# Kernel tuning notes

Hardware: AMD Instinct MI355X
Metric: run time of the kernel (lower is better)

## Reference

```python
import jax, jax.numpy as jnp
import numpy as np
import math

PAD, DIL, K = 4, 2, 3  # causal dilated conv: pad = dilation*(kernel-1)


def _conv1d_causal(x, w, b):
    # x: [B, C, L], w: [O, I, K]
    y = jax.lax.conv_general_dilated(
        x, w, window_strides=(1,), padding=[(PAD, PAD)], rhs_dilation=(DIL,),
        dimension_numbers=('NCH', 'OIH', 'NCH'))
    return (y + b[None, :, None])[:, :, :-PAD]  # trim trailing pad -> length L


def _attn_weights(x, wq, wk):
    # einsum('jj,ijk->ijk', W, X) == diag(W)[None,:,None] * X
    q = jnp.diagonal(wq)[None, :, None] * x
    k = jnp.diagonal(wk)[None, :, None] * x
    scores = jnp.einsum('bnd,bmd->bnm', q, k) / math.sqrt(x.shape[-1])
    return jax.nn.softmax(scores, axis=-1)  # [B, N, N]


def _gcn(x, A, W, b):
    # GCNConv with dense fully-connected edge weights A[r,c] (src r -> dst c):
    # deg[c] = sum_r A[r,c]; out[c] = sum_r A[r,c]/sqrt(deg[r]deg[c]) * (xW)[r] + b
    deg = A.sum(axis=0)
    safe = jnp.where(deg > 0, deg, 1.0)
    dis = jnp.where(deg > 0, 1.0 / jnp.sqrt(safe), 0.0)
    M = dis[:, None] * A * dis[None, :]  # [N, N]
    return jnp.einsum('rc,brh->bch', M, x @ W) + b


def _forward(X_time, conv_w, conv_b, wq_feat, wk_feat, wq_time, wk_time,
             gf1_w, gf1_b, gf2_w, gf2_b, gf3_w, gf3_b,
             gt1_w, gt1_b, gt2_w, gt2_b, gt3_w, gt3_b, proj_w, proj_b):
    B, Wd, F = X_time.shape
    # NOTE: original uses torch.reshape (not transpose) -- replicate exactly.
    X_feat = X_time.reshape(B, F, Wd)
    X_feat = _conv1d_causal(X_feat, conv_w, conv_b)  # [B, F, Wd]

    A_feat = _attn_weights(X_feat, wq_feat, wk_feat).mean(axis=0)  # [F, F]
    h = _gcn(X_feat, A_feat, gf1_w, gf1_b)
    h = _gcn(h, A_feat, gf2_w, gf2_b)
    h = _gcn(h, A_feat, gf3_w, gf3_b)
    out_feat = h.mean(axis=1)  # [B, H]

    A_time = _attn_weights(X_time, wq_time, wk_time).mean(axis=0)  # [Wd, Wd]
    h = _gcn(X_time, A_time, gt1_w, gt1_b)
    h = _gcn(h, A_time, gt2_w, gt2_b)
    h = _gcn(h, A_time, gt3_w, gt3_b)
    out_time = h.mean(axis=1)  # [B, H]

    out = jnp.concatenate([out_feat, out_time], axis=-1) @ proj_w + proj_b
    return out, A_feat.ravel(), A_time.ravel()


def setup_inputs() -> dict:
    B, Wd, F, H, O = 512, 256, 128, 128, 64
    ks = jax.random.split(jax.random.key(0), 20)
    n = lambda k, s, sc=1.0: (jax.random.normal(k, s, dtype=jnp.float32) * sc)
    return {
        'X_time': n(ks[0], (B, Wd, F)),
        'conv_w': n(ks[1], (F, F, K), 0.05), 'conv_b': jnp.zeros((F,), jnp.float32),
        'wq_feat': n(ks[2], (F, F)), 'wk_feat': n(ks[3], (F, F)),
        'wq_time': n(ks[4], (Wd, Wd)), 'wk_time': n(ks[5], (Wd, Wd)),
        'gf1_w': n(ks[6], (Wd, H), 0.05), 'gf1_b': jnp.zeros((H,), jnp.float32),
        'gf2_w': n(ks[7], (H, H), 0.05), 'gf2_b': jnp.zeros((H,), jnp.float32),
        'gf3_w': n(ks[8], (H, H), 0.05), 'gf3_b': jnp.zeros((H,), jnp.float32),
        'gt1_w': n(ks[9], (F, H), 0.05), 'gt1_b': jnp.zeros((H,), jnp.float32),
        'gt2_w': n(ks[10], (H, H), 0.05), 'gt2_b': jnp.zeros((H,), jnp.float32),
        'gt3_w': n(ks[11], (H, H), 0.05), 'gt3_b': jnp.zeros((H,), jnp.float32),
        'proj_w': n(ks[12], (2 * H, O), 0.05), 'proj_b': jnp.zeros((O,), jnp.float32),
    }


def reference(X_time, conv_w, conv_b, wq_feat, wk_feat, wq_time, wk_time,
              gf1_w, gf1_b, gf2_w, gf2_b, gf3_w, gf3_b,
              gt1_w, gt1_b, gt2_w, gt2_b, gt3_w, gt3_b, proj_w, proj_b):
    return _forward(X_time, conv_w, conv_b, wq_feat, wk_feat, wq_time, wk_time,
                    gf1_w, gf1_b, gf2_w, gf2_b, gf3_w, gf3_b,
                    gt1_w, gt1_b, gt2_w, gt2_b, gt3_w, gt3_b, proj_w, proj_b)
```

## Files before the change

### kernel.cpp

```cpp
#include <hip/hip_runtime.h>
#include <hip/hip_bf16.h>

#define NB 512
#define WD 256
#define NF 128

typedef __attribute__((ext_vector_type(8))) short short8v;
typedef __attribute__((ext_vector_type(4))) float f32x4;

__device__ inline unsigned pk2bf(float a, float b) {
  __hip_bfloat162 h;
  h.x = __float2bfloat16(a);
  h.y = __float2bfloat16(b);
  unsigned r;
  __builtin_memcpy(&r, &h, 4);
  return r;
}

__device__ inline float bf2f(unsigned short u) {
  unsigned v = (unsigned)u << 16;
  float f;
  __builtin_memcpy(&f, &v, 4);
  return f;
}

__global__ __launch_bounds__(256) void prep_x(
    const float* __restrict__ X, __hip_bfloat16* __restrict__ Xflat,
    __hip_bfloat16* __restrict__ Xt)
{
  __shared__ float tile[32][33];
  int b = blockIdx.y, tt = blockIdx.x;
  int i0 = (tt >> 3) * 32, l0 = (tt & 7) * 32;
  const float* Xb = X + (size_t)b * 32768;
  __hip_bfloat16* Fb = Xflat + (size_t)b * 32768;
  __hip_bfloat16* Tb = Xt + (size_t)b * 32768;
  int t = threadIdx.x;
  {
    int r = t >> 3, c4 = t & 7;
    float4 v = *(const float4*)(Xb + (size_t)(i0 + r) * 256 + l0 + c4 * 4);
    uint2 p;
    p.x = pk2bf(v.x, v.y);
    p.y = pk2bf(v.z, v.w);
    *(uint2*)(Fb + (size_t)(i0 + r) * 256 + l0 + c4 * 4) = p;
    tile[r][c4 * 4 + 0] = v.x;
    tile[r][c4 * 4 + 1] = v.y;
    tile[r][c4 * 4 + 2] = v.z;
    tile[r][c4 * 4 + 3] = v.w;
  }
  __syncthreads();
  {
    int cr = t >> 3, ch = t & 7;
    float a0 = tile[ch * 4 + 0][cr];
    float a1 = tile[ch * 4 + 1][cr];
    float a2 = tile[ch * 4 + 2][cr];
    float a3 = tile[ch * 4 + 3][cr];
    uint2 q;
    q.x = pk2bf(a0, a1);
    q.y = pk2bf(a2, a3);
    *(uint2*)(Tb + (size_t)(l0 + cr) * 128 + i0 + ch * 4) = q;
  }
}

__global__ void wc_cast(const float* __restrict__ W, __hip_bfloat16* __restrict__ Wc)
{
  int idx = blockIdx.x * 256 + threadIdx.x;
  int o = idx / 384, rem = idx - o * 384;
  int k = rem >> 7, i = rem & 127;
  Wc[idx] = __float2bfloat16(W[(size_t)o * 384 + i * 3 + k]);
}

__global__ __launch_bounds__(256) void conv_gemm(
    const __hip_bfloat16* __restrict__ Xt, const __hip_bfloat16* __restrict__ Wc,
    const float* __restrict__ bias, __hip_bfloat16* __restrict__ Out)
{
  __shared__ unsigned short ldsA[2][4096];
  __shared__ unsigned short ldsB[2][4096];
  int b = blockIdx.y;
  int trt = blockIdx.x;
  int t = threadIdx.x, l = t & 63, w = t >> 6;
  int wr = (w >> 1) * 64, wcc = (w & 1) * 64;
  int lr = l & 15, lg = l >> 4;
  const __hip_bfloat16* Ab = Xt + (size_t)b * 32768;
  f32x4 acc[4][4] = {};

#define CSTAGE(buf, ks)                                                               \
  {                                                                                   \
    int kgrp = (ks) >> 2;                                                             \
    int kk = ((ks) & 3) * 32 + lg * 8;                                                \
    _Pragma("unroll") for (int ff = 0; ff < 2; ++ff) {                                \
      int f = 2 * w + ff;                                                             \
      int lrow = trt * 128 + f * 16 + lr + 2 * kgrp - 4;                              \
      uint4 ga = make_uint4(0, 0, 0, 0);                                              \
      if (lrow >= 0) ga = *(const uint4*)(Ab + (size_t)lrow * 128 + kk);              \
      *(uint4*)&ldsA[buf][f * 512 + l * 8] = ga;                                      \
      *(uint4*)&ldsB[buf][f * 512 + l * 8] =                                          \
          *(const uint4*)(Wc + (size_t)(f * 16 + lr) * 384 + (ks) * 32 + lg * 8);     \
    }                                                                                 \
  }

  CSTAGE(0, 0)
  __syncthreads();
  for (int ks = 0; ks < 12; ++ks) {
    int buf = ks & 1;
    if (ks + 1 < 12) CSTAGE((ks + 1) & 1, ks + 1)
    short8v a[4], bq[4];
#pragma unroll
    for (int i = 0; i < 4; ++i)
      a[i] = *(const short8v*)&ldsA[buf][((wr >> 4) + i) * 512 + l * 8];
#pragma unroll
    for (int j = 0; j < 4; ++j)
      bq[j] = *(const short8v*)&ldsB[buf][((wcc >> 4) + j) * 512 + l * 8];
#pragma unroll
    for (int i = 0; i < 4; ++i)
#pragma unroll
      for (int j = 0; j < 4; ++j)
        acc[i][j] = __builtin_amdgcn_mfma_f32_16x16x32_bf16(a[i], bq[j], acc[i][j], 0, 0, 0);
    __syncthreads();
  }

  __hip_bfloat16* Ob = Out + (size_t)b * 32768;
#pragma unroll
  for (int i = 0; i < 4; ++i) {
#pragma unroll
    for (int j = 0; j < 4; ++j) {
      int r = trt * 128 + wr + i * 16 + lg * 4;
      int c = wcc + j * 16 + lr;
      f32x4 v = acc[i][j];
      float bv = bias[c];
      uint2 p;
      p.x = pk2bf(v[0] + bv, v[1] + bv);
      p.y = pk2bf(v[2] + bv, v[3] + bv);
      *(uint2*)(Ob + (size_t)c * 256 + r) = p;
    }
  }
}

template <int N, int D, int BPG>
__global__ __launch_bounds__(512) void gram_acc(
    const __hip_bfloat16* __restrict__ X, const float* __restrict__ Wq,
    const float* __restrict__ Wk, __hip_bfloat16* __restrict__ partial, float scale)
{
  constexpr int NT = N / 16;
  constexpr int KS = D / 32;
  constexpr int C8 = D / 8;
  __shared__ char lds[N * D * 2];
  int t = threadIdx.x, l = t & 63, w = t >> 6;
  int lr = l & 15, lg = l >> 4;
  int rowbase = blockIdx.x * 128 + w * 16;
  int swz = (lr & 7) << 4;

  float dkr[NT];
#pragma unroll
  for (int m = 0; m < NT; ++m) dkr[m] = Wk[(size_t)(m * 16 + lr) * (N + 1)] * scale;
  float dqr[4];
#pragma unroll
  for (int i = 0; i < 4; ++i) dqr[i] = Wq[(size_t)(rowbase + lg * 4 + i) * (N + 1)];

  float sumA[4][NT] = {};

#pragma unroll 1
  for (int g = 0; g < BPG; ++g) {
    const __hip_bfloat16* Xb = X + (size_t)(blockIdx.y * BPG + g) * N * D;
    __syncthreads();
    for (int chunk = t; chunk < N * C8; chunk += 512) {
      int row = chunk / C8, c8 = chunk - row * C8;
      int off = row * (2 * D) + ((c8 * 16) ^ ((row & 7) << 4));
      *(uint4*)(lds + off) = *(const uint4*)(Xb + (size_t)row * D + c8 * 8);
    }
    __syncthreads();

    f32x4 acc[NT] = {};
#pragma unroll
    for (int ks = 0; ks < KS; ++ks) {
      int coff = (ks * 64 + lg * 16) ^ swz;
      short8v a = *(const short8v*)(lds + (rowbase + lr) * (2 * D) + coff);
#pragma unroll
      for (int m = 0; m < NT; ++m) {
        short8v bb = *(const short8v*)(lds + (m * 16 + lr) * (2 * D) + coff);
        acc[m] = __builtin_amdgcn_mfma_f32_16x16x32_bf16(a, bb, acc[m], 0, 0, 0);
      }
    }

#pragma unroll
    for (int i = 0; i < 4; ++i) {
      float v[NT];
      float mx = -3.0e38f;
#pragma unroll
      for (int m = 0; m < NT; ++m) {
        v[m] = acc[m][i] * dqr[i] * dkr[m];
        mx = fmaxf(mx, v[m]);
      }
#pragma unroll
      for (int off = 1; off < 16; off <<= 1) mx = fmaxf(mx, __shfl_xor(mx, off));
      float sum = 0.f;
#pragma unroll
      for (int m = 0; m < NT; ++m) { v[m] = __expf(v[m] - mx); sum += v[m]; }
#pragma unroll
      for (int off = 1; off < 16; off <<= 1) sum += __shfl_xor(sum, off);
      float inv = 1.0f / sum;
#pragma unroll
      for (int m = 0; m < NT; ++m) sumA[i][m] += v[m] * inv;
    }
  }

  __hip_bfloat16* Pp = partial + (size_t)blockIdx.y * N * N;
#pragma unroll
  for (int i = 0; i < 4; ++i) {
    int row = rowbase + lg * 4 + i;
#pragma unroll
    for (int m = 0; m < NT; ++m)
      Pp[(size_t)row * N + m * 16 + lr] = __float2bfloat16(sumA[i][m]);
  }
}

__global__ __launch_bounds__(256) void reduce_g(
    const __hip_bfloat16* __restrict__ partial, float* __restrict__ l2, int NN, int GS)
{
  int idx = (blockIdx.x * 256 + threadIdx.x) * 8;
  const __hip_bfloat16* p = partial + (size_t)blockIdx.y * GS * NN + idx;
  float a[8] = {};
#pragma unroll 4
  for (int g = 0; g < GS; ++g) {
    uint4 u = *(const uint4*)(p + (size_t)g * NN);
    unsigned arr[4] = {u.x, u.y, u.z, u.w};
#pragma unroll
    for (int q = 0; q < 4; ++q) {
      a[2 * q] += bf2f((unsigned short)(arr[q] & 0xffff));
      a[2 * q + 1] += bf2f((unsigned short)(arr[q] >> 16));
    }
  }
  float* dst = l2 + (size_t)blockIdx.y * NN + idx;
  *(float4*)dst = make_float4(a[0], a[1], a[2], a[3]);
  *(float4*)(dst + 4) = make_float4(a[4], a[5], a[6], a[7]);
}

__global__ void A_fin(const float* __restrict__ partial, float* __restrict__ A1,
                      float* __restrict__ A2, int NN, int G)
{
  int idx = (blockIdx.x * 256 + threadIdx.x) * 4;
  float4 a = make_float4(0.f, 0.f, 0.f, 0.f);
  for (int g = 0; g < G; ++g) {
    float4 v = *(const float4*)(partial + (size_t)g * NN + idx);
    a.x += v.x; a.y += v.y; a.z += v.z; a.w += v.w;
  }
  a.x *= (1.0f / NB); a.y *= (1.0f / NB); a.z *= (1.0f / NB); a.w *= (1.0f / NB);
  *(float4*)(A1 + idx) = a;
  *(float4*)(A2 + idx) = a;
}

__global__ __launch_bounds__(256) void deg_both(
    const float* __restrict__ Af, const float* __restrict__ At,
    float* __restrict__ disf, float* __restrict__ dist)
{
  __shared__ float red[4][64];
  int bid = blockIdx.x;
  int branch = bid >= 2;
  int N = branch ? 256 : 128;
  const float* A = branch ? At : Af;
  float* dis = branch ? dist : disf;
  int cb = (branch ? (bid - 2) : bid) * 64;
  int t = threadIdx.x, lane = t & 63, rg = t >> 6;
  float s = 0.f;
  for (int r = rg; r < N; r += 4) s += A[(size_t)r * N + cb + lane];
  red[rg][lane] = s;
  __syncthreads();
  if (t < 64) {
    float d = red[0][t] + red[1][t] + red[2][t] + red[3][t];
    dis[cb + t] = (d > 0.f) ? (1.0f / sqrtf(d)) : 0.0f;
  }
}

__global__ __launch_bounds__(256) void mv_both(
    const float* __restrict__ Af, const float* __restrict__ At,
    const float* __restrict__ vf, const float* __restrict__ vt,
    const float* __restrict__ disf, const float* __restrict__ dist,
    float* __restrict__ aof, float* __restrict__ aot,
    float* __restrict__ wof, float* __restrict__ wot, int doScale)
{
  int bid = blockIdx.x;
  int branch = bid >= 32;
  int N = branch ? 256 : 128;
  const float* A = branch ? At : Af;
  const float* v = branch ? vt : vf;
  const float* dis = branch ? dist : disf;
  float* ao = branch ? aot : aof;
  float* wo = branch ? wot : wof;
  int r = (branch ? (bid - 32) : bid) * 4 + (threadIdx.x >> 6);
  int lane = threadIdx.x & 63;
  const float* Ar = A + (size_t)r * N;
  float s = 0.f;
  for (int c = lane * 4; c < N; c += 256) {
    float4 av = *(const float4*)(Ar + c);
    s += av.x * v[c] + av.y * v[c + 1] + av.z * v[c + 2] + av.w * v[c + 3];
  }
#pragma unroll
  for (int off = 32; off > 0; off >>= 1) s += __shfl_xor(s, off);
  if (lane == 0) {
    float a = dis[r] * s;
    float scale = doScale ? (branch ? (1.0f / 256.0f) : (1.0f / 128.0f)) : 1.0f;
    ao[r] = a * scale;
    wo[r] = dis[r] * a;
  }
}

__global__ __launch_bounds__(256) void sum_both(
    const float* __restrict__ af, const float* __restrict__ at,
    float* __restrict__ sv, int idx)
{
  __shared__ float part[4];
  int branch = blockIdx.x;
  int N = branch ? 256 : 128;
  const float* a = branch ? at : af;
  int t = threadIdx.x, lane = t & 63, w = t >> 6;
  float x = (t < N) ? a[t] : 0.f;
#pragma unroll
  for (int off = 32; off > 0; off >>= 1) x += __shfl_xor(x, off);
  if (lane == 0) part[w] = x;
  __syncthreads();
  if (t == 0) sv[branch * 2 + idx] = part[0] + part[1] + part[2] + part[3];
}

__global__ __launch_bounds__(256) void qchain(
    const float* __restrict__ Af, const float* __restrict__ At,
    const float* __restrict__ Bf, const float* __restrict__ Bt,
    float* __restrict__ Cf, float* __restrict__ Ct, int Mf, int Mt)
{
  int branch = blockIdx.y;
  const float* A = branch ? At : Af;
  const float* B = branch ? Bt : Bf;
  float* C = branch ? Ct : Cf;
  int M = branch ? Mt : Mf;
  int r = blockIdx.x * 4 + (threadIdx.x >> 6);
  int o = threadIdx.x & 63;
  if (r >= M) return;
  const float* Ar = A + (size_t)r * 128;
  float s = 0.f;
#pragma unroll 8
  for (int k = 0; k < 128; k += 4) {
    float4 wv = *(const float4*)(Ar + k);
    s += wv.x * B[k * 64 + o] + wv.y * B[(k + 1) * 64 + o] +
         wv.z * B[(k + 2) * 64 + o] + wv.w * B[(k + 3) * 64 + o];
  }
  C[(size_t)r * 64 + o] = s;
}

__global__ __launch_bounds__(128) void bias_fold(
    const float* __restrict__ gf1b, const float* __restrict__ gf2w, const float* __restrict__ gf2b,
    const float* __restrict__ gf3w, const float* __restrict__ gf3b,
    const float* __restrict__ gt1b, const float* __restrict__ gt2w, const float* __restrict__ gt2b,
    const float* __restrict__ gt3w, const float* __restrict__ gt3b,
    const float* __restrict__ projw, const float* __restrict__ sv,
    float* __restrict__ cb)
{
  int branch = blockIdx.x;
  int N = branch ? 256 : 128;
  const float* W2 = branch ? gt2w : gf2w;
  const float* W3 = branch ? gt3w : gf3w;
  const float* b1 = branch ? gt1b : gf1b;
  const float* b2 = branch ? gt2b : gf2b;
  const float* b3 = branch ? gt3b : gf3b;
  const float* P = projw + (size_t)branch * 128 * 64;
  float s1 = sv[branch * 2 + 0], s2 = sv[branch * 2 + 1];
  __shared__ float r1[128], cf[128];
  int t = threadIdx.x;

  {
    float s = 0.f;
#pragma unroll 4
    for (int h = 0; h < 128; ++h) s += b1[h] * W2[(size_t)h * 128 + t];
    r1[t] = s;
  }
  __syncthreads();
  {
    float sa = 0.f, sb = 0.f;
#pragma unroll 4
    for (int h = 0; h < 128; ++h) {
      float w3v = W3[(size_t)h * 128 + t];
      sa += r1[h] * w3v;
      sb += b2[h] * w3v;
    }
    cf[t] = (s2 * sa + s1 * sb) * (1.0f / N) + b3[t];
  }
  __syncthreads();
  if (t < 64) {
    float s = 0.f;
#pragma unroll 4
    for (int h = 0; h < 128; ++h) s += cf[h] * P[(size_t)h * 64 + t];
    cb[branch * 64 + t] = s;
  }
}

__global__ __launch_bounds__(256) void gcn_out(
    const __hip_bfloat16* __restrict__ XF, const __hip_bfloat16* __restrict__ Xt,
    const float* __restrict__ uf, const float* __restrict__ ut,
    const float* __restrict__ Qf, const float* __restrict__ Qt,
    const float* __restrict__ cb, const float* __restrict__ pb,
    float* __restrict__ out)
{
  __shared__ float red[2048];
  __shared__ float yfL[256], ytL[128], red3[4][64];
  int b = blockIdx.x, t = threadIdx.x;

  {
    int rr = t >> 5, cc = t & 31;
    const __hip_bfloat16* base = XF + (size_t)b * 32768;
    float acc[8] = {};
    for (int it = 0; it < 16; ++it) {
      int row = it * 8 + rr;
      float uw = uf[row];
      uint4 v = *(const uint4*)(base + (size_t)row * 256 + cc * 8);
      unsigned arr[4] = {v.x, v.y, v.z, v.w};
#pragma unroll
      for (int q = 0; q < 4; ++q) {
        acc[2 * q] += uw * bf2f((unsigned short)(arr[q] & 0xffff));
        acc[2 * q + 1] += uw * bf2f((unsigned short)(arr[q] >> 16));
      }
    }
#pragma unroll
    for (int j = 0; j < 8; ++j) red[rr * 256 + cc * 8 + j] = acc[j];
  }
  __syncthreads();
  {
    float s = 0.f;
#pragma unroll
    for (int g = 0; g < 8; ++g) s += red[g * 256 + t];
    yfL[t] = s;
  }
  __syncthreads();
  {
    int rr = t >> 4, cc = t & 15;
    const __hip_bfloat16* base = Xt + (size_t)b * 32768;
    float acc[8] = {};
    for (int it = 0; it < 16; ++it) {
      int row = it * 16 + rr;
      float uw = ut[row];
      uint4 v = *(const uint4*)(base + (size_t)row * 128 + cc * 8);
      unsigned arr[4] = {v.x, v.y, v.z, v.w};
#pragma unroll
      for (int q = 0; q < 4; ++q) {
        acc[2 * q] += uw * bf2f((unsigned short)(arr[q] & 0xffff));
        acc[2 * q + 1] += uw * bf2f((unsigned short)(arr[q] >> 16));
      }
    }
#pragma unroll
    for (int j = 0; j < 8; ++j) red[rr * 128 + cc * 8 + j] = acc[j];
  }
  __syncthreads();
  if (t < 128) {
    float s = 0.f;
#pragma unroll
    for (int g = 0; g < 16; ++g) s += red[g * 128 + t];
    ytL[t] = s;
  }
  __syncthreads();
  {
    int grp = t >> 6, o = t & 63;
    float s = 0.f;
    for (int jj = 0; jj < 64; ++jj) {
      int j = grp * 64 + jj;
      s += yfL[j] * Qf[(size_t)j * 64 + o];
    }
    for (int jj = 0; jj < 32; ++jj) {
      int j = grp * 32 + jj;
      s += ytL[j] * Qt[(size_t)j * 64 + o];
    }
    red3[grp][o] = s;
  }
  __syncthreads();
  if (t < 64) {
    out[(size_t)b * 64 + t] = red3[0][t] + red3[1][t] + red3[2][t] + red3[3][t] +
                              pb[t] + cb[t] + cb[64 + t];
  }
}

extern "C" void kernel_launch(void* const* d_in, const int* in_sizes, int n_in,
                              void* d_out, int out_size, void* d_ws, size_t ws_size,
                              hipStream_t stream)
{
  const float* X_time = (const float*)d_in[0];
  const float* conv_w = (const float*)d_in[1];
  const float* conv_b = (const float*)d_in[2];
  const float* wq_feat = (const float*)d_in[3];
  const float* wk_feat = (const float*)d_in[4];
  const float* wq_time = (const float*)d_in[5];
  const float* wk_time = (const float*)d_in[6];
  const float* gf1_w = (const float*)d_in[7];
  const float* gf1_b = (const float*)d_in[8];
  const float* gf2_w = (const float*)d_in[9];
  const float* gf2_b = (const float*)d_in[10];
  const float* gf3_w = (const float*)d_in[11];
  const float* gf3_b = (const float*)d_in[12];
  const float* gt1_w = (const float*)d_in[13];
  const float* gt1_b = (const float*)d_in[14];
  const float* gt2_w = (const float*)d_in[15];
  const float* gt2_b = (const float*)d_in[16];
  const float* gt3_w = (const float*)d_in[17];
  const float* gt3_b = (const float*)d_in[18];
  const float* proj_w = (const float*)d_in[19];
  const float* proj_b = (const float*)d_in[20];

  typedef __hip_bfloat16 bf16;
  char* ws = (char*)d_ws;
  const size_t MiB = 1ull << 20;
  bf16* XFb = (bf16*)ws;
  bf16* Xtb = (bf16*)(ws + 34 * MiB);
  bf16* partial_f = (bf16*)(ws + 68 * MiB);
  bf16* partial_t = (bf16*)(ws + 100 * MiB);
  bf16* Xt = (bf16*)(ws + 100 * MiB);
  float* l2f = (float*)(ws + 164 * MiB);
  float* l2t = (float*)(ws + 166 * MiB);
  char* SM = ws + 171 * MiB;
  float* A_feat = (float*)SM;
  float* A_time = (float*)(SM + 65536);
  float* uf = (float*)(SM + 327680);
  float* ut = (float*)(SM + 328704);
  float* sv = (float*)(SM + 329728);
  float* Qf = (float*)(SM + 331776);
  float* Qt = (float*)(SM + 397312);
  float* cb = (float*)(SM + 430080);
  bf16* Wcv = (bf16*)(SM + 432128);
  float* S3f = (float*)(SM + 530432);
  float* S3t = (float*)(SM + 563200);
  float* S2f = (float*)(SM + 595968);
  float* S2t = (float*)(SM + 628736);
  float* dis_f = (float*)(SM + 661504);
  float* dis_t = (float*)(SM + 662528);
  float* a1f = (float*)(SM + 663552);
  float* a1t = (float*)(SM + 664576);
  float* a2f = (float*)(SM + 665600);
  float* a2t = (float*)(SM + 666624);
  float* w1f = (float*)(SM + 667648);
  float* w1t = (float*)(SM + 668672);
  float* w2f = (float*)(SM + 669696);
  float* w2t = (float*)(SM + 670720);
  float* wdf = (float*)(SM + 671744);
  float* wdt = (float*)(SM + 672768);

  float* out = (float*)d_out;
  float* outA_f = out + 32768;
  float* outA_t = out + 49152;

  prep_x<<<dim3(32, NB), 256, 0, stream>>>(X_time, Xtb, Xt);
  wc_cast<<<192, 256, 0, stream>>>(conv_w, Wcv);
  conv_gemm<<<dim3(2, NB), 256, 0, stream>>>(Xt, Wcv, conv_b, XFb);
  gram_acc<128, 256, 1><<<dim3(1, 512), 512, 0, stream>>>(XFb, wq_feat, wk_feat,
                                                          partial_f, 0.0625f);
  gram_acc<256, 128, 2><<<dim3(2, 256), 512, 0, stream>>>(Xtb, wq_time, wk_time,
                                                          partial_t, 0.08838834764831845f);
  reduce_g<<<dim3(8, 16), 256, 0, stream>>>(partial_f, l2f, 16384, 32);
  reduce_g<<<dim3(32, 16), 256, 0, stream>>>(partial_t, l2t, 65536, 16);
  A_fin<<<16, 256, 0, stream>>>(l2f, A_feat, outA_f, 16384, 16);
  A_fin<<<64, 256, 0, stream>>>(l2t, A_time, outA_t, 65536, 16);
  deg_both<<<6, 256, 0, stream>>>(A_feat, A_time, dis_f, dis_t);
  mv_both<<<96, 256, 0, stream>>>(A_feat, A_time, dis_f, dis_t, dis_f, dis_t,
                                  a1f, a1t, w1f, w1t, 0);
  sum_both<<<2, 256, 0, stream>>>(a1f, a1t, sv, 0);
  mv_both<<<96, 256, 0, stream>>>(A_feat, A_time, w1f, w1t, dis_f, dis_t,
                                  a2f, a2t, w2f, w2t, 0);
  sum_both<<<2, 256, 0, stream>>>(a2f, a2t, sv, 1);
  mv_both<<<96, 256, 0, stream>>>(A_feat, A_time, w2f, w2t, dis_f, dis_t,
                                  uf, ut, wdf, wdt, 1);
  qchain<<<dim3(32, 2), 256, 0, stream>>>(gf3_w, gt3_w, proj_w, proj_w + 8192,
                                          S3f, S3t, 128, 128);
  qchain<<<dim3(32, 2), 256, 0, stream>>>(gf2_w, gt2_w, S3f, S3t, S2f, S2t, 128, 128);
  qchain<<<dim3(64, 2), 256, 0, stream>>>(gf1_w, gt1_w, S2f, S2t, Qf, Qt, 256, 128);
  bias_fold<<<2, 128, 0, stream>>>(gf1_b, gf2_w, gf2_b, gf3_w, gf3_b,
                                   gt1_b, gt2_w, gt2_b, gt3_w, gt3_b,
                                   proj_w, sv, cb);
  gcn_out<<<NB, 256, 0, stream>>>(XFb, Xtb, uf, ut, Qf, Qt, cb, proj_b, out);
}
```

Baseline: 213.7 us.

## Double-buffer LDS in gram_acc with register prefetch and more batches per block

gram_acc now keeps two LDS buffers. It loads the next batch's tile into registers while running MFMA and softmax on the current tile, then stores it to the other buffer, so global loads overlap compute and one sync per batch is dropped. Each block now handles twice as many batches, which halves the grid and the number of bf16 partial matrices; the reduce_g and A_fin group counts are adjusted to match. The LDS footprint doubles to 128KB for both instantiations, which limits residency to one block per CU. It also leaves fewer blocks per launch.

```diff
diff --git a/kernel.cpp b/kernel.cpp
--- a/kernel.cpp
+++ b/kernel.cpp
@@ -143,12 +143,21 @@
   constexpr int NT = N / 16;
   constexpr int KS = D / 32;
   constexpr int C8 = D / 8;
-  __shared__ char lds[N * D * 2];
+  __shared__ char lds[2][N * D * 2];
   int t = threadIdx.x, l = t & 63, w = t >> 6;
   int lr = l & 15, lg = l >> 4;
   int rowbase = blockIdx.x * 128 + w * 16;
   int swz = (lr & 7) << 4;
 
+  int srow[8], soff[8];
+#pragma unroll
+  for (int c = 0; c < 8; ++c) {
+    int chunk = c * 512 + t;
+    int row = chunk / C8, c8 = chunk - row * C8;
+    srow[c] = row * D + c8 * 8;
+    soff[c] = row * (2 * D) + ((c8 * 16) ^ ((row & 7) << 4));
+  }
+
   float dkr[NT];
 #pragma unroll
   for (int m = 0; m < NT; ++m) dkr[m] = Wk[(size_t)(m * 16 + lr) * (N + 1)] * scale;
@@ -158,25 +167,34 @@
 
   float sumA[4][NT] = {};
 
+  {
+    const __hip_bfloat16* Xb = X + (size_t)(blockIdx.y * BPG) * N * D;
+    uint4 r[8];
+#pragma unroll
+    for (int c = 0; c < 8; ++c) r[c] = *(const uint4*)(Xb + srow[c]);
+#pragma unroll
+    for (int c = 0; c < 8; ++c) *(uint4*)(lds[0] + soff[c]) = r[c];
+  }
+  __syncthreads();
+
 #pragma unroll 1
   for (int g = 0; g < BPG; ++g) {
-    const __hip_bfloat16* Xb = X + (size_t)(blockIdx.y * BPG + g) * N * D;
-    __syncthreads();
-    for (int chunk = t; chunk < N * C8; chunk += 512) {
-      int row = chunk / C8, c8 = chunk - row * C8;
-      int off = row * (2 * D) + ((c8 * 16) ^ ((row & 7) << 4));
-      *(uint4*)(lds + off) = *(const uint4*)(Xb + (size_t)row * D + c8 * 8);
-    }
-    __syncthreads();
+    char* cur = lds[g & 1];
+    uint4 rn[8];
+    if (g + 1 < BPG) {
+      const __hip_bfloat16* Xb = X + (size_t)(blockIdx.y * BPG + g + 1) * N * D;
+#pragma unroll
+      for (int c = 0; c < 8; ++c) rn[c] = *(const uint4*)(Xb + srow[c]);
+    }
 
     f32x4 acc[NT] = {};
 #pragma unroll
     for (int ks = 0; ks < KS; ++ks) {
       int coff = (ks * 64 + lg * 16) ^ swz;
-      short8v a = *(const short8v*)(lds + (rowbase + lr) * (2 * D) + coff);
+      short8v a = *(const short8v*)(cur + (rowbase + lr) * (2 * D) + coff);
 #pragma unroll
       for (int m = 0; m < NT; ++m) {
-        short8v bb = *(const short8v*)(lds + (m * 16 + lr) * (2 * D) + coff);
+        short8v bb = *(const short8v*)(cur + (m * 16 + lr) * (2 * D) + coff);
         acc[m] = __builtin_amdgcn_mfma_f32_16x16x32_bf16(a, bb, acc[m], 0, 0, 0);
       }
     }
@@ -200,6 +218,13 @@
       float inv = 1.0f / sum;
 #pragma unroll
       for (int m = 0; m < NT; ++m) sumA[i][m] += v[m] * inv;
+    }
+
+    if (g + 1 < BPG) {
+      char* nxt = lds[(g + 1) & 1];
+#pragma unroll
+      for (int c = 0; c < 8; ++c) *(uint4*)(nxt + soff[c]) = rn[c];
+      __syncthreads();
     }
   }
 
@@ -543,14 +568,14 @@
   prep_x<<<dim3(32, NB), 256, 0, stream>>>(X_time, Xtb, Xt);
   wc_cast<<<192, 256, 0, stream>>>(conv_w, Wcv);
   conv_gemm<<<dim3(2, NB), 256, 0, stream>>>(Xt, Wcv, conv_b, XFb);
-  gram_acc<128, 256, 1><<<dim3(1, 512), 512, 0, stream>>>(XFb, wq_feat, wk_feat,
+  gram_acc<128, 256, 2><<<dim3(1, 256), 512, 0, stream>>>(XFb, wq_feat, wk_feat,
                                                           partial_f, 0.0625f);
-  gram_acc<256, 128, 2><<<dim3(2, 256), 512, 0, stream>>>(Xtb, wq_time, wk_time,
+  gram_acc<256, 128, 4><<<dim3(2, 128), 512, 0, stream>>>(Xtb, wq_time, wk_time,
                                                           partial_t, 0.08838834764831845f);
-  reduce_g<<<dim3(8, 16), 256, 0, stream>>>(partial_f, l2f, 16384, 32);
-  reduce_g<<<dim3(32, 16), 256, 0, stream>>>(partial_t, l2t, 65536, 16);
+  reduce_g<<<dim3(8, 16), 256, 0, stream>>>(partial_f, l2f, 16384, 16);
+  reduce_g<<<dim3(32, 8), 256, 0, stream>>>(partial_t, l2t, 65536, 16);
   A_fin<<<16, 256, 0, stream>>>(l2f, A_feat, outA_f, 16384, 16);
-  A_fin<<<64, 256, 0, stream>>>(l2t, A_time, outA_t, 65536, 16);
+  A_fin<<<64, 256, 0, stream>>>(l2t, A_time, outA_t, 65536, 8);
   deg_both<<<6, 256, 0, stream>>>(A_feat, A_time, dis_f, dis_t);
   mv_both<<<96, 256, 0, stream>>>(A_feat, A_time, dis_f, dis_t, dis_f, dis_t,
                                   a1f, a1t, w1f, w1t, 0);
```

New measurement: 208.1 us. -2.6%, faster.

## Double-buffer gram tiles via async global_load_lds and merge reduction launches

Applied to the files above, without the earlier changes.

The gram kernel now stages each batch tile straight into LDS with global_load_lds into a double buffer, prefetching the next batch while MFMA and softmax run on the current one. Each block handles twice as many batches, which halves the partial buffers, and the diagonal scale vector moves from registers into LDS. The separate feat/time reduce and finalize launches are merged into one launch each. The cost is doubled LDS use per block (occupancy of 1), fewer blocks in flight, and an extra LDS read in the softmax loop.

```diff
diff --git a/kernel.cpp b/kernel.cpp
--- a/kernel.cpp
+++ b/kernel.cpp
@@ -136,47 +136,57 @@
 }
 
 template <int N, int D, int BPG>
-__global__ __launch_bounds__(512) void gram_acc(
+__global__ __launch_bounds__(512, 1) void gram_acc(
     const __hip_bfloat16* __restrict__ X, const float* __restrict__ Wq,
     const float* __restrict__ Wk, __hip_bfloat16* __restrict__ partial, float scale)
 {
   constexpr int NT = N / 16;
   constexpr int KS = D / 32;
   constexpr int C8 = D / 8;
-  __shared__ char lds[N * D * 2];
+  __shared__ char lds[2][N * D * 2];
+  __shared__ float ldsD[N];
   int t = threadIdx.x, l = t & 63, w = t >> 6;
   int lr = l & 15, lg = l >> 4;
   int rowbase = blockIdx.x * 128 + w * 16;
   int swz = (lr & 7) << 4;
 
-  float dkr[NT];
-#pragma unroll
-  for (int m = 0; m < NT; ++m) dkr[m] = Wk[(size_t)(m * 16 + lr) * (N + 1)] * scale;
+  if (t < N) ldsD[t] = Wk[(size_t)t * (N + 1)] * scale;
   float dqr[4];
 #pragma unroll
   for (int i = 0; i < 4; ++i) dqr[i] = Wq[(size_t)(rowbase + lg * 4 + i) * (N + 1)];
 
   float sumA[4][NT] = {};
+
+#define GSTAGE(buf, gb)                                                             \
+  {                                                                                 \
+    const __hip_bfloat16* Xb_ = (gb);                                               \
+    _Pragma("unroll") for (int c = 0; c < 8; ++c) {                                 \
+      int chunk = c * 512 + t;                                                      \
+      int row_ = chunk / C8, j_ = chunk % C8;                                       \
+      int gsrc = row_ * D + ((j_ ^ (row_ & 7)) << 3);                               \
+      __builtin_amdgcn_global_load_lds(                                             \
+          (const __attribute__((address_space(1))) unsigned int*)(const void*)(Xb_ + gsrc), \
+          (__attribute__((address_space(3))) unsigned int*)(void*)(&lds[buf][chunk * 16]),  \
+          16, 0, 0);                                                                \
+    }                                                                               \
+  }
+
+  GSTAGE(0, X + (size_t)(blockIdx.y * BPG) * N * D)
+  __syncthreads();
 
 #pragma unroll 1
   for (int g = 0; g < BPG; ++g) {
-    const __hip_bfloat16* Xb = X + (size_t)(blockIdx.y * BPG + g) * N * D;
-    __syncthreads();
-    for (int chunk = t; chunk < N * C8; chunk += 512) {
-      int row = chunk / C8, c8 = chunk - row * C8;
-      int off = row * (2 * D) + ((c8 * 16) ^ ((row & 7) << 4));
-      *(uint4*)(lds + off) = *(const uint4*)(Xb + (size_t)row * D + c8 * 8);
-    }
-    __syncthreads();
+    if (g + 1 < BPG) GSTAGE((g + 1) & 1, X + (size_t)(blockIdx.y * BPG + g + 1) * N * D)
+    const char* cur = lds[g & 1];
 
     f32x4 acc[NT] = {};
 #pragma unroll
     for (int ks = 0; ks < KS; ++ks) {
       int coff = (ks * 64 + lg * 16) ^ swz;
-      short8v a = *(const short8v*)(lds + (rowbase + lr) * (2 * D) + coff);
+      short8v a = *(const short8v*)(cur + (rowbase + lr) * (2 * D) + coff);
 #pragma unroll
       for (int m = 0; m < NT; ++m) {
-        short8v bb = *(const short8v*)(lds + (m * 16 + lr) * (2 * D) + coff);
+        short8v bb = *(const short8v*)(cur + (m * 16 + lr) * (2 * D) + coff);
         acc[m] = __builtin_amdgcn_mfma_f32_16x16x32_bf16(a, bb, acc[m], 0, 0, 0);
       }
     }
@@ -187,7 +197,7 @@
       float mx = -3.0e38f;
 #pragma unroll
       for (int m = 0; m < NT; ++m) {
-        v[m] = acc[m][i] * dqr[i] * dkr[m];
+        v[m] = acc[m][i] * dqr[i] * ldsD[m * 16 + lr];
         mx = fmaxf(mx, v[m]);
       }
 #pragma unroll
@@ -201,6 +211,8 @@
 #pragma unroll
       for (int m = 0; m < NT; ++m) sumA[i][m] += v[m] * inv;
     }
+
+    if (g + 1 < BPG) __syncthreads();
   }
 
   __hip_bfloat16* Pp = partial + (size_t)blockIdx.y * N * N;
@@ -213,14 +225,21 @@
   }
 }
 
-__global__ __launch_bounds__(256) void reduce_g(
-    const __hip_bfloat16* __restrict__ partial, float* __restrict__ l2, int NN, int GS)
-{
-  int idx = (blockIdx.x * 256 + threadIdx.x) * 8;
-  const __hip_bfloat16* p = partial + (size_t)blockIdx.y * GS * NN + idx;
+__global__ __launch_bounds__(256) void reduce_g2(
+    const __hip_bfloat16* __restrict__ pf, const __hip_bfloat16* __restrict__ pt,
+    float* __restrict__ l2f, float* __restrict__ l2t)
+{
+  int bid = blockIdx.x;
+  const __hip_bfloat16* partial;
+  float* l2;
+  int NN, bx, gy;
+  if (bid < 128) { partial = pf; l2 = l2f; NN = 16384; bx = bid & 7; gy = bid >> 3; }
+  else { int r2 = bid - 128; partial = pt; l2 = l2t; NN = 65536; bx = r2 & 31; gy = r2 >> 5; }
+  int idx = (bx * 256 + threadIdx.x) * 8;
+  const __hip_bfloat16* p = partial + (size_t)gy * 16 * NN + idx;
   float a[8] = {};
 #pragma unroll 4
-  for (int g = 0; g < GS; ++g) {
+  for (int g = 0; g < 16; ++g) {
     uint4 u = *(const uint4*)(p + (size_t)g * NN);
     unsigned arr[4] = {u.x, u.y, u.z, u.w};
 #pragma unroll
@@ -229,18 +248,26 @@
       a[2 * q + 1] += bf2f((unsigned short)(arr[q] >> 16));
     }
   }
-  float* dst = l2 + (size_t)blockIdx.y * NN + idx;
+  float* dst = l2 + (size_t)gy * NN + idx;
   *(float4*)dst = make_float4(a[0], a[1], a[2], a[3]);
   *(float4*)(dst + 4) = make_float4(a[4], a[5], a[6], a[7]);
 }
 
-__global__ void A_fin(const float* __restrict__ partial, float* __restrict__ A1,
-                      float* __restrict__ A2, int NN, int G)
-{
-  int idx = (blockIdx.x * 256 + threadIdx.x) * 4;
+__global__ __launch_bounds__(256) void A_fin2(
+    const float* __restrict__ l2f, const float* __restrict__ l2t,
+    float* __restrict__ A1f, float* __restrict__ A1t,
+    float* __restrict__ A2f, float* __restrict__ A2t)
+{
+  int bid = blockIdx.x;
+  const float* src;
+  float *A1, *A2;
+  int NN, G, ib;
+  if (bid < 16) { src = l2f; A1 = A1f; A2 = A2f; NN = 16384; G = 16; ib = bid; }
+  else { src = l2t; A1 = A1t; A2 = A2t; NN = 65536; G = 8; ib = bid - 16; }
+  int idx = (ib * 256 + threadIdx.x) * 4;
   float4 a = make_float4(0.f, 0.f, 0.f, 0.f);
   for (int g = 0; g < G; ++g) {
-    float4 v = *(const float4*)(partial + (size_t)g * NN + idx);
+    float4 v = *(const float4*)(src + (size_t)g * NN + idx);
     a.x += v.x; a.y += v.y; a.z += v.z; a.w += v.w;
   }
   a.x *= (1.0f / NB); a.y *= (1.0f / NB); a.z *= (1.0f / NB); a.w *= (1.0f / NB);
@@ -543,14 +570,12 @@
   prep_x<<<dim3(32, NB), 256, 0, stream>>>(X_time, Xtb, Xt);
   wc_cast<<<192, 256, 0, stream>>>(conv_w, Wcv);
   conv_gemm<<<dim3(2, NB), 256, 0, stream>>>(Xt, Wcv, conv_b, XFb);
-  gram_acc<128, 256, 1><<<dim3(1, 512), 512, 0, stream>>>(XFb, wq_feat, wk_feat,
+  gram_acc<128, 256, 2><<<dim3(1, 256), 512, 0, stream>>>(XFb, wq_feat, wk_feat,
                                                           partial_f, 0.0625f);
-  gram_acc<256, 128, 2><<<dim3(2, 256), 512, 0, stream>>>(Xtb, wq_time, wk_time,
+  gram_acc<256, 128, 4><<<dim3(2, 128), 512, 0, stream>>>(Xtb, wq_time, wk_time,
                                                           partial_t, 0.08838834764831845f);
-  reduce_g<<<dim3(8, 16), 256, 0, stream>>>(partial_f, l2f, 16384, 32);
-  reduce_g<<<dim3(32, 16), 256, 0, stream>>>(partial_t, l2t, 65536, 16);
-  A_fin<<<16, 256, 0, stream>>>(l2f, A_feat, outA_f, 16384, 16);
-  A_fin<<<64, 256, 0, stream>>>(l2t, A_time, outA_t, 65536, 16);
+  reduce_g2<<<384, 256, 0, stream>>>(partial_f, partial_t, l2f, l2t);
+  A_fin2<<<80, 256, 0, stream>>>(l2f, l2t, A_feat, A_time, outA_f, outA_t);
   deg_both<<<6, 256, 0, stream>>>(A_feat, A_time, dis_f, dis_t);
   mv_both<<<96, 256, 0, stream>>>(A_feat, A_time, dis_f, dis_t, dis_f, dis_t,
                                   a1f, a1t, w1f, w1t, 0);
```

Result: faster. 190.7 us (-10.7%).
